# Optimization experiments

Hardware: AMD Instinct MI355X
Metric: run time of the kernel (lower is better)

The kernel has to match this reference:

```python
import jax, jax.numpy as jnp
import numpy as np

B, N, D = 4, 4096, 768
SCALE = 1.0 / np.sqrt(D).astype(np.float32)


def setup_inputs() -> dict:
    key = jax.random.key(0)
    k1, k2, k3 = jax.random.split(key, 3)
    x = jax.random.normal(k1, (B, N, D), dtype=jnp.float32)
    w_qkv = jax.random.normal(k2, (D, 3 * D), dtype=jnp.float32) * (1.0 / np.sqrt(D))
    b_qkv = jnp.zeros((3 * D,), dtype=jnp.float32)
    w_out = jax.random.normal(k3, (D, D), dtype=jnp.float32) * (1.0 / np.sqrt(D))
    b_out = jnp.zeros((D,), dtype=jnp.float32)
    return {"x": x, "w_qkv": w_qkv, "b_qkv": b_qkv, "w_out": w_out, "b_out": b_out}


def reference(x, w_qkv, b_qkv, w_out, b_out):
    # fused QKV projection: [B,N,3D]
    qkv = jnp.einsum("bnd,de->bne", x, w_qkv) + b_qkv
    q, k, v = jnp.split(qkv, 3, axis=-1)          # each [B,N,D]
    # scaled dot-product attention (single head)
    scores = jnp.einsum("bnd,bmd->bnm", q, k) * SCALE  # [B,N,N]
    attn = jax.nn.softmax(scores, axis=-1)
    ctx = jnp.einsum("bnm,bmd->bnd", attn, v)          # [B,N,D]
    out = jnp.einsum("bnd,de->bne", ctx, w_out) + b_out
    return out
```

## Files before the change

### kernel.cpp

```cpp
#include <hip/hip_runtime.h>
#include <cstdint>
#include <cstddef>

#define BB 4
#define NN 4096
#define DD 768
#define EE 2304
#define MTOT 16384
static constexpr float ATT_SCALE = 0.03608439182435161f;

typedef _Float16 v8h __attribute__((ext_vector_type(8)));
typedef _Float16 v4h __attribute__((ext_vector_type(4)));
typedef float v4f __attribute__((ext_vector_type(4)));

__device__ __forceinline__ void async_copy16(void* lds, const void* gmem) {
  __builtin_amdgcn_global_load_lds(
      (const __attribute__((address_space(1))) uint32_t*)(uintptr_t)gmem,
      (__attribute__((address_space(3))) uint32_t*)(uintptr_t)lds,
      16, 0, 0);
}

#define VM_WAIT(n) asm volatile("s_waitcnt vmcnt(" #n ")" ::: "memory")
#define LGKM0 asm volatile("s_waitcnt lgkmcnt(0)" ::: "memory")
#define SCHED0 __builtin_amdgcn_sched_barrier(0)
#define BAR __builtin_amdgcn_s_barrier()

enum { EPI_QKV = 0, EPI_F16 = 1, EPI_OUT = 2, EPI_PV = 3 };

template <int EPI, int SWZ = 0>
__global__ __launch_bounds__(512, 2) void gemm256(
    const _Float16* __restrict__ A, int lda, size_t zA,
    const _Float16* __restrict__ Bt, int ldb, size_t zB,
    int K,
    float* __restrict__ c_f32,
    _Float16* __restrict__ c_f16,
    int ldc, size_t zC, size_t chalf,
    const float* __restrict__ bias,
    _Float16* __restrict__ q_out,
    _Float16* __restrict__ k_out,
    _Float16* __restrict__ v_out) {
  __shared__ __align__(16) _Float16 As[2][2][256 * 32];
  __shared__ __align__(16) _Float16 Bs[2][2][256 * 32];

  const int tid = threadIdx.x;
  const int wid = tid >> 6, lane = tid & 63;
  const int wr = wid >> 2, wc = wid & 3;
  const int lq = lane >> 4, lr = lane & 15;

  int bx = blockIdx.x, by = blockIdx.y;
  if constexpr (SWZ == 1) {
    const int lin = bx + gridDim.x * by;
    const int xcd = lin & 7, j = lin >> 3;
    const int stc = gridDim.x >> 3;
    bx = (xcd % stc) * 8 + (j & 7);
    by = (xcd / stc) * 4 + ((j >> 3) & 3) + (j >> 5) * 4 * (8 / stc == 0 ? 1 : (gridDim.y / 4 / (8 / stc) == 0 ? 1 : (gridDim.y / 4) / (gridDim.y / 4)));
  }
  const int m0 = bx * 256, n0 = by * 256;
  const int z = blockIdx.z;
  int bidx, koff;
  if constexpr (EPI == EPI_PV) {
    bidx = z & 1;
    koff = (z >> 1) * K;
  } else {
    bidx = z;
    koff = 0;
  }

  const _Float16* Ab = A + (size_t)bidx * zA + (size_t)m0 * lda + koff;
  const _Float16* Bb = Bt + (size_t)bidx * zB + (size_t)n0 * ldb + koff;

  const int c0 = tid, c1 = tid + 512;
  const int r0 = c0 >> 2, r1 = c1 >> 2;
  const int k0c = ((c0 & 3) ^ ((r0 >> 1) & 3)) << 3;
  const int k1c = ((c1 & 3) ^ ((r1 >> 1) & 3)) << 3;
  const size_t ga0 = (size_t)r0 * lda + k0c, ga1 = (size_t)r1 * lda + k1c;
  const size_t gb0 = (size_t)r0 * ldb + k0c, gb1 = (size_t)r1 * ldb + k1c;

  int aoff[8], boff[4];
#pragma unroll
  for (int t = 0; t < 8; ++t) {
    const int ra = wr * 128 + t * 16 + lr;
    aoff[t] = ra * 32 + ((lq ^ ((ra >> 1) & 3)) << 3);
  }
#pragma unroll
  for (int n = 0; n < 4; ++n) {
    const int rb = wc * 64 + n * 16 + lr;
    boff[n] = rb * 32 + ((lq ^ ((rb >> 1) & 3)) << 3);
  }

  v4f acc[8][4] = {};
  const int NT = K / 64;

  auto stageA = [&](int slot, int ks, int kt) {
    const _Float16* s = Ab + (size_t)(kt * 64 + ks * 32);
    async_copy16(&As[slot][ks][(size_t)c0 * 8], s + ga0);
    async_copy16(&As[slot][ks][(size_t)c1 * 8], s + ga1);
  };
  auto stageB = [&](int slot, int ks, int kt) {
    const _Float16* s = Bb + (size_t)(kt * 64 + ks * 32);
    async_copy16(&Bs[slot][ks][(size_t)c0 * 8], s + gb0);
    async_copy16(&Bs[slot][ks][(size_t)c1 * 8], s + gb1);
  };
  auto mfma16 = [&](const v8h* af_, const v8h* bf_, int mbase) {
#pragma unroll
    for (int mt = 0; mt < 4; ++mt)
#pragma unroll
      for (int nt = 0; nt < 4; ++nt)
        acc[mbase + mt][nt] = __builtin_amdgcn_mfma_f32_16x16x32_f16(
            af_[mt], bf_[nt], acc[mbase + mt][nt], 0, 0, 0);
  };

  stageA(0, 0, 0);
  stageB(0, 0, 0);
  stageA(0, 1, 0);
  stageB(0, 1, 0);

  for (int t = 0; t < NT; ++t) {
    const int slot = t & 1, ns = slot ^ 1;
    const bool pre = (t + 1 < NT);
    const _Float16* A0s = &As[slot][0][0];
    const _Float16* B0s = &Bs[slot][0][0];
    const _Float16* A1s = &As[slot][1][0];
    const _Float16* B1s = &Bs[slot][1][0];

    v8h a_[4], b0_[4], b1_[4];

    if (pre) {
      stageA(ns, 0, t + 1);
      VM_WAIT(6);
    } else {
      VM_WAIT(4);
    }
    SCHED0;
    BAR;
    SCHED0;
#pragma unroll
    for (int i = 0; i < 4; ++i) a_[i] = *(const v8h*)(A0s + aoff[i]);
#pragma unroll
    for (int i = 0; i < 4; ++i) b0_[i] = *(const v8h*)(B0s + boff[i]);
    __builtin_amdgcn_s_setprio(1);
    mfma16(a_, b0_, 0);
    __builtin_amdgcn_s_setprio(0);

    if (pre) stageB(ns, 0, t + 1);
#pragma unroll
    for (int i = 0; i < 4; ++i) a_[i] = *(const v8h*)(A0s + aoff[4 + i]);
    __builtin_amdgcn_s_setprio(1);
    mfma16(a_, b0_, 4);
    __builtin_amdgcn_s_setprio(0);

    if (pre) {
      stageA(ns, 1, t + 1);
      VM_WAIT(6);
    } else {
      VM_WAIT(0);
    }
    SCHED0;
    BAR;
    SCHED0;
#pragma unroll
    for (int i = 0; i < 4; ++i) a_[i] = *(const v8h*)(A1s + aoff[i]);
#pragma unroll
    for (int i = 0; i < 4; ++i) b1_[i] = *(const v8h*)(B1s + boff[i]);
    __builtin_amdgcn_s_setprio(1);
    mfma16(a_, b1_, 0);
    __builtin_amdgcn_s_setprio(0);

    if (pre) stageB(ns, 1, t + 1);
#pragma unroll
    for (int i = 0; i < 4; ++i) a_[i] = *(const v8h*)(A1s + aoff[4 + i]);
    __builtin_amdgcn_s_setprio(1);
    mfma16(a_, b1_, 4);
    __builtin_amdgcn_s_setprio(0);

    LGKM0;
    SCHED0;
    BAR;
    SCHED0;
  }

  float* cf = nullptr;
  _Float16* ch = nullptr;
  if constexpr (EPI == EPI_PV)
    cf = c_f32 + (size_t)(z >> 1) * chalf + (size_t)bidx * zC;
  else if constexpr (EPI == EPI_OUT)
    cf = c_f32 + (size_t)bidx * zC;
  else if constexpr (EPI == EPI_F16)
    ch = c_f16 + (size_t)bidx * zC;

#pragma unroll
  for (int mt = 0; mt < 8; ++mt) {
#pragma unroll
    for (int nt = 0; nt < 4; ++nt) {
#pragma unroll
      for (int rg = 0; rg < 4; ++rg) {
        const int gm = m0 + wr * 128 + mt * 16 + lq * 4 + rg;
        const int gn = n0 + wc * 64 + nt * 16 + lr;
        float v = acc[mt][nt][rg];
        if constexpr (EPI == EPI_QKV) {
          v += bias[gn];
          if (gn < DD) {
            q_out[(size_t)gm * DD + gn] = (_Float16)(v * ATT_SCALE);
          } else if (gn < 2 * DD) {
            k_out[(size_t)gm * DD + (gn - DD)] = (_Float16)v;
          } else {
            v_out[(size_t)gm * DD + (gn - 2 * DD)] = (_Float16)v;
          }
        } else if constexpr (EPI == EPI_F16) {
          ch[(size_t)gm * ldc + gn] = (_Float16)v;
        } else {
          cf[(size_t)gm * ldc + gn] = (EPI == EPI_OUT) ? v + bias[gn] : v;
        }
      }
    }
  }
}

__global__ __launch_bounds__(256) void reduce_ctx(const float* __restrict__ h0,
                                                  const float* __restrict__ h1,
                                                  _Float16* __restrict__ out,
                                                  int n4) {
  int i = blockIdx.x * blockDim.x + threadIdx.x;
  if (i < n4) {
    v4f a = ((const v4f*)h0)[i];
    v4f b = ((const v4f*)h1)[i];
    v4h o;
#pragma unroll
    for (int j = 0; j < 4; ++j) o[j] = (_Float16)(a[j] + b[j]);
    ((v4h*)out)[i] = o;
  }
}

__global__ __launch_bounds__(256) void softmax_rows_f16(_Float16* __restrict__ S) {
  _Float16* row = S + (size_t)blockIdx.y * NN * NN + (size_t)blockIdx.x * NN;
  const int tid = threadIdx.x;
  const int lane = tid & 63, wid = tid >> 6;

  float f[16];
  float m = -3.0e38f;
#pragma unroll
  for (int i = 0; i < 2; ++i) {
    v8h v = ((const v8h*)row)[tid + i * 256];
#pragma unroll
    for (int j = 0; j < 8; ++j) {
      f[i * 8 + j] = (float)v[j];
      m = fmaxf(m, f[i * 8 + j]);
    }
  }
#pragma unroll
  for (int off = 32; off > 0; off >>= 1) m = fmaxf(m, __shfl_xor(m, off));
  __shared__ float redm[4], reds[4];
  if (lane == 0) redm[wid] = m;
  __syncthreads();
  m = fmaxf(fmaxf(redm[0], redm[1]), fmaxf(redm[2], redm[3]));

  float sum = 0.f;
#pragma unroll
  for (int i = 0; i < 16; ++i) {
    f[i] = __expf(f[i] - m);
    sum += f[i];
  }
#pragma unroll
  for (int off = 32; off > 0; off >>= 1) sum += __shfl_xor(sum, off);
  if (lane == 0) reds[wid] = sum;
  __syncthreads();
  sum = reds[0] + reds[1] + reds[2] + reds[3];
  const float inv = 1.0f / sum;
#pragma unroll
  for (int i = 0; i < 2; ++i) {
    v8h o;
#pragma unroll
    for (int j = 0; j < 8; ++j) o[j] = (_Float16)(f[i * 8 + j] * inv);
    ((v8h*)row)[tid + i * 256] = o;
  }
}

__global__ __launch_bounds__(256) void cvt_f16(const float* __restrict__ in,
                                               _Float16* __restrict__ out, int n4) {
  int i = blockIdx.x * blockDim.x + threadIdx.x;
  if (i < n4) {
    v4f v = ((const v4f*)in)[i];
    v4h o;
#pragma unroll
    for (int j = 0; j < 4; ++j) o[j] = (_Float16)v[j];
    ((v4h*)out)[i] = o;
  }
}

__global__ __launch_bounds__(256) void transpose_cvt(const float* __restrict__ in,
                                                     _Float16* __restrict__ out,
                                                     int R, int C) {
  __shared__ float tile[32][33];
  const int bx = blockIdx.x * 32;
  const int by = blockIdx.y * 32;
  const int tx = threadIdx.x & 31, ty = threadIdx.x >> 5;
#pragma unroll
  for (int i = 0; i < 32; i += 8)
    tile[ty + i][tx] = in[(size_t)(by + ty + i) * C + (bx + tx)];
  __syncthreads();
#pragma unroll
  for (int i = 0; i < 32; i += 8)
    out[(size_t)(bx + ty + i) * R + (by + tx)] = (_Float16)tile[tx][ty + i];
}

__global__ __launch_bounds__(256) void transpose_v(const _Float16* __restrict__ in,
                                                   _Float16* __restrict__ out) {
  __shared__ _Float16 tile[32][33];
  const int b = blockIdx.z;
  const _Float16* src = in + (size_t)b * NN * DD;
  _Float16* dst = out + (size_t)b * NN * DD;
  const int bx = blockIdx.x * 32;
  const int by = blockIdx.y * 32;
  const int tx = threadIdx.x & 31, ty = threadIdx.x >> 5;
#pragma unroll
  for (int i = 0; i < 32; i += 8)
    tile[ty + i][tx] = src[(size_t)(by + ty + i) * DD + (bx + tx)];
  __syncthreads();
#pragma unroll
  for (int i = 0; i < 32; i += 8)
    dst[(size_t)(bx + ty + i) * NN + (by + tx)] = tile[tx][ty + i];
}

extern "C" void kernel_launch(void* const* d_in, const int* in_sizes, int n_in,
                              void* d_out, int out_size, void* d_ws, size_t ws_size,
                              hipStream_t stream) {
  const float* x = (const float*)d_in[0];
  const float* w_qkv = (const float*)d_in[1];
  const float* b_qkv = (const float*)d_in[2];
  const float* w_out = (const float*)d_in[3];
  const float* b_out = (const float*)d_in[4];
  float* out = (float*)d_out;
  char* ws = (char*)d_ws;

  _Float16* xh    = (_Float16*)(ws + 0);
  _Float16* wqkvh = (_Float16*)(ws + 25165824);
  _Float16* wouth = (_Float16*)(ws + 28704768);
  _Float16* Qh    = (_Float16*)(ws + 29884416);
  _Float16* Kh    = (_Float16*)(ws + 55050240);
  _Float16* Vh    = (_Float16*)(ws + 80216064);
  _Float16* Sh    = (_Float16*)(ws + 105381888);
  _Float16* Vth   = (_Float16*)(ws + 0);
  _Float16* Ch    = (_Float16*)(ws + 80216064);

  const size_t zQK = (size_t)NN * DD;
  const size_t zS = (size_t)NN * NN;
  const size_t zCtx = (size_t)NN * DD;
  const size_t chalf = 2 * zCtx;

  cvt_f16<<<dim3((MTOT * DD / 4) / 256), 256, 0, stream>>>(x, xh, MTOT * DD / 4);
  transpose_cvt<<<dim3(EE / 32, DD / 32), 256, 0, stream>>>(w_qkv, wqkvh, DD, EE);
  transpose_cvt<<<dim3(DD / 32, DD / 32), 256, 0, stream>>>(w_out, wouth, DD, DD);

  gemm256<EPI_QKV><<<dim3(MTOT / 256, EE / 256), 512, 0, stream>>>(
      xh, DD, 0, wqkvh, DD, 0, DD, nullptr, nullptr, 0, 0, 0, b_qkv, Qh, Kh, Vh);

  transpose_v<<<dim3(DD / 32, NN / 32, BB), 256, 0, stream>>>(Vh, Vth);

  for (int c = 0; c < BB / 2; ++c) {
    const _Float16* Qc = Qh + (size_t)c * 2 * zQK;
    const _Float16* Kc = Kh + (size_t)c * 2 * zQK;
    const _Float16* Vtc = Vth + (size_t)c * 2 * zQK;
    gemm256<EPI_F16, 1><<<dim3(NN / 256, NN / 256, 2), 512, 0, stream>>>(
        Qc, DD, zQK, Kc, DD, zQK, DD, nullptr, Sh, NN, zS, 0, nullptr, nullptr,
        nullptr, nullptr);
    softmax_rows_f16<<<dim3(NN, 2), 256, 0, stream>>>(Sh);
    gemm256<EPI_PV><<<dim3(NN / 256, DD / 256, 4), 512, 0, stream>>>(
        Sh, NN, zS, Vtc, NN, zQK, NN / 2, out, nullptr, DD, zCtx, chalf,
        nullptr, nullptr, nullptr, nullptr);
    reduce_ctx<<<dim3((int)(chalf / 4 / 256)), 256, 0, stream>>>(
        out, out + chalf, Ch + (size_t)c * 2 * zQK, (int)(chalf / 4));
  }

  gemm256<EPI_OUT><<<dim3(MTOT / 256, DD / 256), 512, 0, stream>>>(
      Ch, DD, 0, wouth, DD, 0, DD, out, nullptr, DD, 0, 0, b_out, nullptr,
      nullptr, nullptr);
}
```

Measured before the change: 543.9 us.

## Restructure GEMM main loop into ping-pong barrier phases with early LDS reads

The GEMM k-loop is reorganised so each half-tile phase first issues its LDS fragment reads, then the next async global-to-LDS prefetch, then a barrier and lgkm wait before the MFMA block, with an extra barrier after each MFMA block. This is meant to keep the two wave groups alternating between memory and MFMA work so LDS reads and global loads overlap with matrix math. The XCD-aware block swizzle is also simplified to hardcoded shifts that assume a 16-wide grid in x. The extra barriers add synchronisation cost, and the hardcoded swizzle is only correct for the specific grid shapes that use it.

```diff
diff --git a/kernel.cpp b/kernel.cpp
--- a/kernel.cpp
+++ b/kernel.cpp
@@ -49,11 +49,10 @@
 
   int bx = blockIdx.x, by = blockIdx.y;
   if constexpr (SWZ == 1) {
-    const int lin = bx + gridDim.x * by;
+    const int lin = bx + (by << 4);
     const int xcd = lin & 7, j = lin >> 3;
-    const int stc = gridDim.x >> 3;
-    bx = (xcd % stc) * 8 + (j & 7);
-    by = (xcd / stc) * 4 + ((j >> 3) & 3) + (j >> 5) * 4 * (8 / stc == 0 ? 1 : (gridDim.y / 4 / (8 / stc) == 0 ? 1 : (gridDim.y / 4) / (gridDim.y / 4)));
+    bx = (xcd & 1) * 8 + (j & 7);
+    by = (xcd >> 1) * 4 + (j >> 3);
   }
   const int m0 = bx * 256, n0 = by * 256;
   const int z = blockIdx.z;
@@ -114,6 +113,10 @@
   stageB(0, 0, 0);
   stageA(0, 1, 0);
   stageB(0, 1, 0);
+  VM_WAIT(4);
+  SCHED0;
+  BAR;
+  SCHED0;
 
   for (int t = 0; t < NT; ++t) {
     const int slot = t & 1, ns = slot ^ 1;
@@ -125,55 +128,72 @@
 
     v8h a_[4], b0_[4], b1_[4];
 
-    if (pre) {
-      stageA(ns, 0, t + 1);
-      VM_WAIT(6);
-    } else {
-      VM_WAIT(4);
-    }
-    SCHED0;
-    BAR;
-    SCHED0;
 #pragma unroll
     for (int i = 0; i < 4; ++i) a_[i] = *(const v8h*)(A0s + aoff[i]);
 #pragma unroll
     for (int i = 0; i < 4; ++i) b0_[i] = *(const v8h*)(B0s + boff[i]);
+    if (pre) stageA(ns, 0, t + 1);
+    SCHED0;
+    BAR;
+    LGKM0;
+    SCHED0;
     __builtin_amdgcn_s_setprio(1);
     mfma16(a_, b0_, 0);
     __builtin_amdgcn_s_setprio(0);
-
+    SCHED0;
+    BAR;
+    SCHED0;
+
+#pragma unroll
+    for (int i = 0; i < 4; ++i) a_[i] = *(const v8h*)(A0s + aoff[4 + i]);
     if (pre) stageB(ns, 0, t + 1);
-#pragma unroll
-    for (int i = 0; i < 4; ++i) a_[i] = *(const v8h*)(A0s + aoff[4 + i]);
+    SCHED0;
+    if (pre) {
+      VM_WAIT(4);
+    } else {
+      VM_WAIT(0);
+    }
+    SCHED0;
+    BAR;
+    LGKM0;
+    SCHED0;
     __builtin_amdgcn_s_setprio(1);
     mfma16(a_, b0_, 4);
     __builtin_amdgcn_s_setprio(0);
-
-    if (pre) {
-      stageA(ns, 1, t + 1);
-      VM_WAIT(6);
-    } else {
-      VM_WAIT(0);
-    }
-    SCHED0;
-    BAR;
-    SCHED0;
+    SCHED0;
+    BAR;
+    SCHED0;
+
 #pragma unroll
     for (int i = 0; i < 4; ++i) a_[i] = *(const v8h*)(A1s + aoff[i]);
 #pragma unroll
     for (int i = 0; i < 4; ++i) b1_[i] = *(const v8h*)(B1s + boff[i]);
+    if (pre) stageA(ns, 1, t + 1);
+    SCHED0;
+    BAR;
+    LGKM0;
+    SCHED0;
     __builtin_amdgcn_s_setprio(1);
     mfma16(a_, b1_, 0);
     __builtin_amdgcn_s_setprio(0);
-
+    SCHED0;
+    BAR;
+    SCHED0;
+
+#pragma unroll
+    for (int i = 0; i < 4; ++i) a_[i] = *(const v8h*)(A1s + aoff[4 + i]);
     if (pre) stageB(ns, 1, t + 1);
-#pragma unroll
-    for (int i = 0; i < 4; ++i) a_[i] = *(const v8h*)(A1s + aoff[4 + i]);
+    SCHED0;
+    if (pre) {
+      VM_WAIT(4);
+    }
+    SCHED0;
+    BAR;
+    LGKM0;
+    SCHED0;
     __builtin_amdgcn_s_setprio(1);
     mfma16(a_, b1_, 4);
     __builtin_amdgcn_s_setprio(0);
-
-    LGKM0;
     SCHED0;
     BAR;
     SCHED0;
```

Measured after the change: 569.2 us. 1.05x slower.

## Add 128x128 single-buffered GEMM kernel for QKV, PV and output projections

Applied to the files above, without the earlier changes.

Introduces a gemm128 kernel (256 threads, 128x128 tile, K-step 64, swizzled LDS, single buffer) and uses it for the QKV projection, PV product and output projection in place of the 256x256 double-buffered kernel. The smaller tile raises the number of blocks on the grid, which matters for the narrow-N GEMMs (D=768) where 256 tiles leave the GPU under-filled. In exchange it gives up double buffering and load/compute overlap, and the epilogue writes are strided scalar stores. The QK swizzle is also simplified to hardcoded grid constants.

```diff
diff --git a/kernel.cpp b/kernel.cpp
--- a/kernel.cpp
+++ b/kernel.cpp
@@ -26,6 +26,110 @@
 #define BAR __builtin_amdgcn_s_barrier()
 
 enum { EPI_QKV = 0, EPI_F16 = 1, EPI_OUT = 2, EPI_PV = 3 };
+
+template <int EPI>
+__global__ __launch_bounds__(256) void gemm128(
+    const _Float16* __restrict__ A, int lda, size_t zA,
+    const _Float16* __restrict__ Bt, int ldb, size_t zB,
+    int K,
+    float* __restrict__ c_f32,
+    _Float16* __restrict__ c_f16,
+    int ldc, size_t zC, size_t chalf,
+    const float* __restrict__ bias,
+    _Float16* __restrict__ q_out,
+    _Float16* __restrict__ k_out,
+    _Float16* __restrict__ v_out) {
+  __shared__ __align__(16) _Float16 As[128 * 64 + 3072];
+  __shared__ __align__(16) _Float16 Bs[128 * 64 + 3072];
+
+  const int tid = threadIdx.x;
+  const int wid = tid >> 6, lane = tid & 63;
+  const int wr = wid >> 1, wc = wid & 1;
+  const int lq = lane >> 4, lr = lane & 15;
+  const int m0 = blockIdx.x * 128, n0 = blockIdx.y * 128;
+  const int z = blockIdx.z;
+  int bidx, koff;
+  if constexpr (EPI == EPI_PV) {
+    bidx = z & 1;
+    koff = (z >> 1) * K;
+  } else {
+    bidx = z;
+    koff = 0;
+  }
+
+  const _Float16* Ab = A + (size_t)bidx * zA + (size_t)m0 * lda + koff;
+  const _Float16* Bb = Bt + (size_t)bidx * zB + (size_t)n0 * ldb + koff;
+
+  v4f acc[4][4] = {};
+
+  for (int k0 = 0; k0 < K; k0 += 64) {
+#pragma unroll
+    for (int i = 0; i < 4; ++i) {
+      const int c = i * 256 + tid;
+      const int r = c >> 3;
+      const int kc = (c & 7) ^ (r & 7);
+      async_copy16(As + (size_t)c * 8, Ab + (size_t)r * lda + (k0 + kc * 8));
+      async_copy16(Bs + (size_t)c * 8, Bb + (size_t)r * ldb + (k0 + kc * 8));
+    }
+    __syncthreads();
+
+#pragma unroll
+    for (int ks = 0; ks < 2; ++ks) {
+      v8h af[4], bf[4];
+#pragma unroll
+      for (int t = 0; t < 4; ++t) {
+        const int ra = wr * 64 + t * 16 + lr;
+        const int rb = wc * 64 + t * 16 + lr;
+        const int cb = ks * 4 + lq;
+        af[t] = *(const v8h*)(As + ra * 64 + (((cb ^ (ra & 7)) << 3)));
+        bf[t] = *(const v8h*)(Bs + rb * 64 + (((cb ^ (rb & 7)) << 3)));
+      }
+#pragma unroll
+      for (int mt = 0; mt < 4; ++mt)
+#pragma unroll
+        for (int nt = 0; nt < 4; ++nt)
+          acc[mt][nt] = __builtin_amdgcn_mfma_f32_16x16x32_f16(
+              af[mt], bf[nt], acc[mt][nt], 0, 0, 0);
+    }
+    __syncthreads();
+  }
+
+  float* cf = nullptr;
+  _Float16* ch = nullptr;
+  if constexpr (EPI == EPI_PV)
+    cf = c_f32 + (size_t)(z >> 1) * chalf + (size_t)bidx * zC;
+  else if constexpr (EPI == EPI_OUT)
+    cf = c_f32 + (size_t)bidx * zC;
+  else if constexpr (EPI == EPI_F16)
+    ch = c_f16 + (size_t)bidx * zC;
+
+#pragma unroll
+  for (int mt = 0; mt < 4; ++mt) {
+#pragma unroll
+    for (int nt = 0; nt < 4; ++nt) {
+#pragma unroll
+      for (int rg = 0; rg < 4; ++rg) {
+        const int gm = m0 + wr * 64 + mt * 16 + lq * 4 + rg;
+        const int gn = n0 + wc * 64 + nt * 16 + lr;
+        float v = acc[mt][nt][rg];
+        if constexpr (EPI == EPI_QKV) {
+          v += bias[gn];
+          if (gn < DD) {
+            q_out[(size_t)gm * DD + gn] = (_Float16)(v * ATT_SCALE);
+          } else if (gn < 2 * DD) {
+            k_out[(size_t)gm * DD + (gn - DD)] = (_Float16)v;
+          } else {
+            v_out[(size_t)gm * DD + (gn - 2 * DD)] = (_Float16)v;
+          }
+        } else if constexpr (EPI == EPI_F16) {
+          ch[(size_t)gm * ldc + gn] = (_Float16)v;
+        } else {
+          cf[(size_t)gm * ldc + gn] = (EPI == EPI_OUT) ? v + bias[gn] : v;
+        }
+      }
+    }
+  }
+}
 
 template <int EPI, int SWZ = 0>
 __global__ __launch_bounds__(512, 2) void gemm256(
@@ -49,11 +153,10 @@
 
   int bx = blockIdx.x, by = blockIdx.y;
   if constexpr (SWZ == 1) {
-    const int lin = bx + gridDim.x * by;
+    const int lin = bx + (by << 4);
     const int xcd = lin & 7, j = lin >> 3;
-    const int stc = gridDim.x >> 3;
-    bx = (xcd % stc) * 8 + (j & 7);
-    by = (xcd / stc) * 4 + ((j >> 3) & 3) + (j >> 5) * 4 * (8 / stc == 0 ? 1 : (gridDim.y / 4 / (8 / stc) == 0 ? 1 : (gridDim.y / 4) / (gridDim.y / 4)));
+    bx = (xcd & 1) * 8 + (j & 7);
+    by = (xcd >> 1) * 4 + (j >> 3);
   }
   const int m0 = bx * 256, n0 = by * 256;
   const int z = blockIdx.z;
@@ -351,7 +454,7 @@
   transpose_cvt<<<dim3(EE / 32, DD / 32), 256, 0, stream>>>(w_qkv, wqkvh, DD, EE);
   transpose_cvt<<<dim3(DD / 32, DD / 32), 256, 0, stream>>>(w_out, wouth, DD, DD);
 
-  gemm256<EPI_QKV><<<dim3(MTOT / 256, EE / 256), 512, 0, stream>>>(
+  gemm128<EPI_QKV><<<dim3(MTOT / 128, EE / 128), 256, 0, stream>>>(
       xh, DD, 0, wqkvh, DD, 0, DD, nullptr, nullptr, 0, 0, 0, b_qkv, Qh, Kh, Vh);
 
   transpose_v<<<dim3(DD / 32, NN / 32, BB), 256, 0, stream>>>(Vh, Vth);
@@ -364,14 +467,14 @@
         Qc, DD, zQK, Kc, DD, zQK, DD, nullptr, Sh, NN, zS, 0, nullptr, nullptr,
         nullptr, nullptr);
     softmax_rows_f16<<<dim3(NN, 2), 256, 0, stream>>>(Sh);
-    gemm256<EPI_PV><<<dim3(NN / 256, DD / 256, 4), 512, 0, stream>>>(
+    gemm128<EPI_PV><<<dim3(NN / 128, DD / 128, 4), 256, 0, stream>>>(
         Sh, NN, zS, Vtc, NN, zQK, NN / 2, out, nullptr, DD, zCtx, chalf,
         nullptr, nullptr, nullptr, nullptr);
     reduce_ctx<<<dim3((int)(chalf / 4 / 256)), 256, 0, stream>>>(
         out, out + chalf, Ch + (size_t)c * 2 * zQK, (int)(chalf / 4));
   }
 
-  gemm256<EPI_OUT><<<dim3(MTOT / 256, DD / 256), 512, 0, stream>>>(
+  gemm128<EPI_OUT><<<dim3(MTOT / 128, DD / 128), 256, 0, stream>>>(
       Ch, DD, 0, wouth, DD, 0, DD, out, nullptr, DD, 0, 0, b_out, nullptr,
       nullptr, nullptr);
 }
```

Measured after the change: 579.4 us. 6.5% more time.

## Replace async global-to-LDS copies with register-staged prefetch and 64-wide K tiles

Applied to the files above, without the earlier changes.

Drops the direct global_load_lds async copies and split 32-wide K sub-buffers. Global tiles are now loaded into registers two iterations ahead and written to a double-buffered 256x64 LDS tile with an 8-way XOR swizzle. This leaves one barrier per K step instead of three. The SWZ block remap is also hardcoded for a 16-wide grid. The cost is extra VGPRs for staging and an extra trip through registers, which may hurt occupancy at launch bounds (512,2).

```diff
diff --git a/kernel.cpp b/kernel.cpp
--- a/kernel.cpp
+++ b/kernel.cpp
@@ -12,15 +12,8 @@
 typedef _Float16 v8h __attribute__((ext_vector_type(8)));
 typedef _Float16 v4h __attribute__((ext_vector_type(4)));
 typedef float v4f __attribute__((ext_vector_type(4)));
-
-__device__ __forceinline__ void async_copy16(void* lds, const void* gmem) {
-  __builtin_amdgcn_global_load_lds(
-      (const __attribute__((address_space(1))) uint32_t*)(uintptr_t)gmem,
-      (__attribute__((address_space(3))) uint32_t*)(uintptr_t)lds,
-      16, 0, 0);
-}
-
-#define VM_WAIT(n) asm volatile("s_waitcnt vmcnt(" #n ")" ::: "memory")
+typedef uint32_t v4u __attribute__((ext_vector_type(4)));
+
 #define LGKM0 asm volatile("s_waitcnt lgkmcnt(0)" ::: "memory")
 #define SCHED0 __builtin_amdgcn_sched_barrier(0)
 #define BAR __builtin_amdgcn_s_barrier()
@@ -39,8 +32,8 @@
     _Float16* __restrict__ q_out,
     _Float16* __restrict__ k_out,
     _Float16* __restrict__ v_out) {
-  __shared__ __align__(16) _Float16 As[2][2][256 * 32];
-  __shared__ __align__(16) _Float16 Bs[2][2][256 * 32];
+  __shared__ __align__(16) _Float16 As[2][256 * 64];
+  __shared__ __align__(16) _Float16 Bs[2][256 * 64];
 
   const int tid = threadIdx.x;
   const int wid = tid >> 6, lane = tid & 63;
@@ -49,11 +42,10 @@
 
   int bx = blockIdx.x, by = blockIdx.y;
   if constexpr (SWZ == 1) {
-    const int lin = bx + gridDim.x * by;
+    const int lin = bx + (by << 4);
     const int xcd = lin & 7, j = lin >> 3;
-    const int stc = gridDim.x >> 3;
-    bx = (xcd % stc) * 8 + (j & 7);
-    by = (xcd / stc) * 4 + ((j >> 3) & 3) + (j >> 5) * 4 * (8 / stc == 0 ? 1 : (gridDim.y / 4 / (8 / stc) == 0 ? 1 : (gridDim.y / 4) / (gridDim.y / 4)));
+    bx = (xcd & 1) * 8 + (j & 7);
+    by = (xcd >> 1) * 4 + (j >> 3);
   }
   const int m0 = bx * 256, n0 = by * 256;
   const int z = blockIdx.z;
@@ -69,37 +61,48 @@
   const _Float16* Ab = A + (size_t)bidx * zA + (size_t)m0 * lda + koff;
   const _Float16* Bb = Bt + (size_t)bidx * zB + (size_t)n0 * ldb + koff;
 
-  const int c0 = tid, c1 = tid + 512;
-  const int r0 = c0 >> 2, r1 = c1 >> 2;
-  const int k0c = ((c0 & 3) ^ ((r0 >> 1) & 3)) << 3;
-  const int k1c = ((c1 & 3) ^ ((r1 >> 1) & 3)) << 3;
-  const size_t ga0 = (size_t)r0 * lda + k0c, ga1 = (size_t)r1 * lda + k1c;
-  const size_t gb0 = (size_t)r0 * ldb + k0c, gb1 = (size_t)r1 * ldb + k1c;
+  int gA[4], gB[4], lds_off[4];
+#pragma unroll
+  for (int i = 0; i < 4; ++i) {
+    const int c = i * 512 + tid;
+    const int r = c >> 3, kc = c & 7;
+    gA[i] = r * lda + kc * 8;
+    gB[i] = r * ldb + kc * 8;
+    lds_off[i] = r * 64 + ((kc ^ (r & 7)) << 3);
+  }
 
   int aoff[8], boff[4];
 #pragma unroll
   for (int t = 0; t < 8; ++t) {
     const int ra = wr * 128 + t * 16 + lr;
-    aoff[t] = ra * 32 + ((lq ^ ((ra >> 1) & 3)) << 3);
+    aoff[t] = ra * 64 + ((lq ^ (ra & 7)) << 3);
   }
 #pragma unroll
   for (int n = 0; n < 4; ++n) {
     const int rb = wc * 64 + n * 16 + lr;
-    boff[n] = rb * 32 + ((lq ^ ((rb >> 1) & 3)) << 3);
+    boff[n] = rb * 64 + ((lq ^ (rb & 7)) << 3);
   }
 
   v4f acc[8][4] = {};
   const int NT = K / 64;
 
-  auto stageA = [&](int slot, int ks, int kt) {
-    const _Float16* s = Ab + (size_t)(kt * 64 + ks * 32);
-    async_copy16(&As[slot][ks][(size_t)c0 * 8], s + ga0);
-    async_copy16(&As[slot][ks][(size_t)c1 * 8], s + ga1);
+  v4u va[4], vb[4];
+
+  auto loadT = [&](int kt) {
+    const _Float16* a = Ab + kt * 64;
+    const _Float16* b = Bb + kt * 64;
+#pragma unroll
+    for (int i = 0; i < 4; ++i) {
+      va[i] = *(const v4u*)(a + gA[i]);
+      vb[i] = *(const v4u*)(b + gB[i]);
+    }
   };
-  auto stageB = [&](int slot, int ks, int kt) {
-    const _Float16* s = Bb + (size_t)(kt * 64 + ks * 32);
-    async_copy16(&Bs[slot][ks][(size_t)c0 * 8], s + gb0);
-    async_copy16(&Bs[slot][ks][(size_t)c1 * 8], s + gb1);
+  auto writeT = [&](int slot) {
+#pragma unroll
+    for (int i = 0; i < 4; ++i) {
+      *(v4u*)(&As[slot][0] + lds_off[i]) = va[i];
+      *(v4u*)(&Bs[slot][0] + lds_off[i]) = vb[i];
+    }
   };
   auto mfma16 = [&](const v8h* af_, const v8h* bf_, int mbase) {
 #pragma unroll
@@ -110,69 +113,52 @@
             af_[mt], bf_[nt], acc[mbase + mt][nt], 0, 0, 0);
   };
 
-  stageA(0, 0, 0);
-  stageB(0, 0, 0);
-  stageA(0, 1, 0);
-  stageB(0, 1, 0);
+  loadT(0);
+  writeT(0);
+  loadT(1);
+  LGKM0;
+  SCHED0;
+  BAR;
+  SCHED0;
 
   for (int t = 0; t < NT; ++t) {
-    const int slot = t & 1, ns = slot ^ 1;
-    const bool pre = (t + 1 < NT);
-    const _Float16* A0s = &As[slot][0][0];
-    const _Float16* B0s = &Bs[slot][0][0];
-    const _Float16* A1s = &As[slot][1][0];
-    const _Float16* B1s = &Bs[slot][1][0];
-
+    const int cur = t & 1, ns = cur ^ 1;
+    const _Float16* Ac = &As[cur][0];
+    const _Float16* Bc = &Bs[cur][0];
     v8h a_[4], b0_[4], b1_[4];
 
-    if (pre) {
-      stageA(ns, 0, t + 1);
-      VM_WAIT(6);
-    } else {
-      VM_WAIT(4);
-    }
-    SCHED0;
-    BAR;
-    SCHED0;
-#pragma unroll
-    for (int i = 0; i < 4; ++i) a_[i] = *(const v8h*)(A0s + aoff[i]);
-#pragma unroll
-    for (int i = 0; i < 4; ++i) b0_[i] = *(const v8h*)(B0s + boff[i]);
+#pragma unroll
+    for (int i = 0; i < 4; ++i) a_[i] = *(const v8h*)(Ac + aoff[i]);
+#pragma unroll
+    for (int i = 0; i < 4; ++i) b0_[i] = *(const v8h*)(Bc + boff[i]);
     __builtin_amdgcn_s_setprio(1);
     mfma16(a_, b0_, 0);
     __builtin_amdgcn_s_setprio(0);
 
-    if (pre) stageB(ns, 0, t + 1);
-#pragma unroll
-    for (int i = 0; i < 4; ++i) a_[i] = *(const v8h*)(A0s + aoff[4 + i]);
+#pragma unroll
+    for (int i = 0; i < 4; ++i) a_[i] = *(const v8h*)(Ac + aoff[4 + i]);
     __builtin_amdgcn_s_setprio(1);
     mfma16(a_, b0_, 4);
     __builtin_amdgcn_s_setprio(0);
 
-    if (pre) {
-      stageA(ns, 1, t + 1);
-      VM_WAIT(6);
-    } else {
-      VM_WAIT(0);
-    }
-    SCHED0;
-    BAR;
-    SCHED0;
-#pragma unroll
-    for (int i = 0; i < 4; ++i) a_[i] = *(const v8h*)(A1s + aoff[i]);
-#pragma unroll
-    for (int i = 0; i < 4; ++i) b1_[i] = *(const v8h*)(B1s + boff[i]);
+#pragma unroll
+    for (int i = 0; i < 4; ++i) a_[i] = *(const v8h*)(Ac + (aoff[i] ^ 32));
+#pragma unroll
+    for (int i = 0; i < 4; ++i) b1_[i] = *(const v8h*)(Bc + (boff[i] ^ 32));
     __builtin_amdgcn_s_setprio(1);
     mfma16(a_, b1_, 0);
     __builtin_amdgcn_s_setprio(0);
 
-    if (pre) stageB(ns, 1, t + 1);
-#pragma unroll
-    for (int i = 0; i < 4; ++i) a_[i] = *(const v8h*)(A1s + aoff[4 + i]);
+#pragma unroll
+    for (int i = 0; i < 4; ++i) a_[i] = *(const v8h*)(Ac + (aoff[4 + i] ^ 32));
     __builtin_amdgcn_s_setprio(1);
     mfma16(a_, b1_, 4);
     __builtin_amdgcn_s_setprio(0);
 
+    if (t + 1 < NT) {
+      writeT(ns);
+      if (t + 2 < NT) loadT(t + 2);
+    }
     LGKM0;
     SCHED0;
     BAR;
```

New measurement: 546.4 us, median of 2. About the same (+0.5%).
